# Kernel optimization log

Hardware: AMD Instinct MI355X
Metric: run time of the kernel (lower is better)

The kernel has to match this reference:

```python
import jax, jax.numpy as jnp
import numpy as np


def _hungarian(cost):
    """Jonker-Volgenant shortest-augmenting-path LAP solver (minimum cost).

    Returns col_ind such that rows arange(n) are matched to columns col_ind,
    identical (in objective) to scipy.optimize.linear_sum_assignment.
    Runs on host numpy, mirroring the original's detach().cpu() + scipy path.
    """
    cost = np.asarray(cost, dtype=np.float64)
    n = cost.shape[0]
    INF = np.inf
    u = np.zeros(n + 1)
    v = np.zeros(n + 1)
    p = np.zeros(n + 1, dtype=np.int64)   # p[j]: row (1-based) assigned to column j
    way = np.zeros(n + 1, dtype=np.int64)
    for i in range(1, n + 1):
        p[0] = i
        j0 = 0
        minv = np.full(n + 1, INF)
        used = np.zeros(n + 1, dtype=bool)
        while True:
            used[j0] = True
            i0 = p[j0]
            # vectorized relaxation of reduced costs for all unused columns
            cur = cost[i0 - 1] - u[i0] - v[1:]
            free = ~used[1:]
            upd = free & (cur < minv[1:])
            minv[1:] = np.where(upd, cur, minv[1:])
            way[1:] = np.where(upd, j0, way[1:])
            cand = np.where(free, minv[1:], INF)
            j1 = int(np.argmin(cand)) + 1
            delta = cand[j1 - 1]
            u[p[used]] += delta
            v[used] -= delta
            minv[1:] = np.where(free, minv[1:] - delta, minv[1:])
            j0 = j1
            if p[j0] == 0:
                break
        # augment along the alternating path
        while j0:
            j1 = way[j0]
            p[j0] = p[j1]
            j0 = j1
    col = np.empty(n, dtype=np.int64)
    col[p[1:] - 1] = np.arange(n)
    return col


def setup_inputs() -> dict:
    key = jax.random.key(0)
    B, N = 64, 256
    D = jax.random.normal(key, (B, N, N), dtype=jnp.float32)
    return {"D": D}


def reference(D):
    # Host round-trip for the assignment, exactly as the torch module does
    # (D.detach().cpu().numpy() -> scipy LAP per batch element).
    Dn = np.asarray(jax.device_get(D))
    cols = np.stack([_hungarian(Dn[b]) for b in range(Dn.shape[0])])  # [B, N]
    idx = jnp.asarray(cols)[:, :, None]                               # [B, N, 1]
    # gather matched costs D[b, i, col[b, i]] and reduce: mean per batch, then mean
    matched = jnp.take_along_axis(D, idx, axis=2)[..., 0]             # [B, N]
    return matched.mean(axis=1).mean()
```

## Files before the change

kernel.cpp:

```cpp
#include <hip/hip_runtime.h>

#define N_DIM 256
#define BATCH 64
#define BS 64
#define SCALE 4096.0f

#define DPP_MINU(x, ctrl) do {                                                 \
    unsigned _s = (unsigned)__builtin_amdgcn_update_dpp((int)(x), (int)(x),    \
                                                        (ctrl), 0xf, 0xf, false); \
    (x) = ((x) < _s) ? (x) : _s;                                               \
} while (0)

__device__ __forceinline__ unsigned wave_min_u32(unsigned x) {
    DPP_MINU(x, 0x111);
    DPP_MINU(x, 0x112);
    DPP_MINU(x, 0x114);
    DPP_MINU(x, 0x118);
    const unsigned a = (unsigned)__builtin_amdgcn_readlane((int)x, 15);
    const unsigned b = (unsigned)__builtin_amdgcn_readlane((int)x, 31);
    const unsigned c = (unsigned)__builtin_amdgcn_readlane((int)x, 47);
    const unsigned d = (unsigned)__builtin_amdgcn_readlane((int)x, 63);
    const unsigned ab = (a < b) ? a : b;
    const unsigned cd = (c < d) ? c : d;
    return (ab < cd) ? ab : cd;
}

__device__ __forceinline__ int rd4_i(int x0, int x1, int x2, int x3, int idx) {
    const int sel = idx & 3, src = idx >> 2;
    int ab = (sel & 1) ? x1 : x0;
    int cd = (sel & 1) ? x3 : x2;
    int vv = (sel & 2) ? cd : ab;
    return __builtin_amdgcn_readlane(vv, src);
}

#define SET4(x0, x1, x2, x3, idx, val) do {                                    \
    const int _sel = (idx) & 3;                                                \
    if (t == ((idx) >> 2)) {                                                   \
        if (_sel == 0) x0 = (val); else if (_sel == 1) x1 = (val);             \
        else if (_sel == 2) x2 = (val); else x3 = (val);                       \
    }                                                                          \
} while (0)

#define SET_GUARD(idx) do {                                                    \
    if (t == ((idx) >> 2)) {                                                   \
        const int _s = (idx) & 3;                                              \
        if (_s == 0) g0 = 0x7FFFFFFF; else if (_s == 1) g1 = 0x7FFFFFFF;       \
        else if (_s == 2) g2 = 0x7FFFFFFF; else g3 = 0x7FFFFFFF;               \
    }                                                                          \
} while (0)

#define RELAX(hh, addv, predrow) do {                                          \
    int r_, kn_;                                                               \
    r_  = (addv) + lo16((hh).x) + vn0;                                         \
    kn_ = (r_ << 8) | c0i; if (kn_ < k0) { p0 = (predrow); k0 = kn_; }         \
    r_  = (addv) + hi16((hh).x) + vn1;                                         \
    kn_ = (r_ << 8) | c1i; if (kn_ < k1) { p1 = (predrow); k1 = kn_; }         \
    r_  = (addv) + lo16((hh).y) + vn2;                                         \
    kn_ = (r_ << 8) | c2i; if (kn_ < k2) { p2 = (predrow); k2 = kn_; }         \
    r_  = (addv) + hi16((hh).y) + vn3;                                         \
    kn_ = (r_ << 8) | c3i; if (kn_ < k3) { p3 = (predrow); k3 = kn_; }         \
} while (0)

__device__ __forceinline__ int lo16(int p) { return (int)(short)(p & 0xFFFF); }
__device__ __forceinline__ int hi16(int p) { return p >> 16; }

__global__ __launch_bounds__(BS) void lap_kernel(const float* __restrict__ Dm,
                                                 double* __restrict__ batch_sums) {
    const int b = blockIdx.x;
    const int t = threadIdx.x;
    const float* __restrict__ cost = Dm + (size_t)b * N_DIM * N_DIM;
    const float4* __restrict__ cost4 = (const float4*)cost;

    __shared__ int2     chi[N_DIM * BS];
    __shared__ int      u_s[N_DIM];
    __shared__ int      v_s[N_DIM];
    __shared__ int      row4col_s[N_DIM];
    __shared__ int      col4row_s[N_DIM];
    __shared__ int      queue_s[N_DIM];
    __shared__ unsigned bid_s[N_DIM];
    __shared__ int      qcnt_s;

    const int c0i = 4 * t, c1i = 4 * t + 1, c2i = 4 * t + 2, c3i = 4 * t + 3;

    int cmn0 = INT_MAX, cmn1 = INT_MAX, cmn2 = INT_MAX, cmn3 = INT_MAX;
    int ca0 = 0, ca1 = 0, ca2 = 0, ca3 = 0;
    for (int r = 0; r < N_DIM; ++r) {
        const float4 c4 = cost4[r * BS + t];
        const int a0 = __float2int_rn(c4.x * SCALE);
        const int a1 = __float2int_rn(c4.y * SCALE);
        const int a2 = __float2int_rn(c4.z * SCALE);
        const int a3 = __float2int_rn(c4.w * SCALE);
        int2 p;
        p.x = (a0 & 0xFFFF) | (a1 << 16);
        p.y = (a2 & 0xFFFF) | (a3 << 16);
        chi[r * BS + t] = p;
        if (a0 < cmn0) { cmn0 = a0; ca0 = r; }
        if (a1 < cmn1) { cmn1 = a1; ca1 = r; }
        if (a2 < cmn2) { cmn2 = a2; ca2 = r; }
        if (a3 < cmn3) { cmn3 = a3; ca3 = r; }
    }
    {
        int4 vv; vv.x = cmn0; vv.y = cmn1; vv.z = cmn2; vv.w = cmn3;
        ((int4*)v_s)[t] = vv;
        int4 zz; zz.x = 0; zz.y = 0; zz.z = 0; zz.w = 0;
        ((int4*)u_s)[t] = zz;
        int4 mm; mm.x = -1; mm.y = -1; mm.z = -1; mm.w = -1;
        ((int4*)row4col_s)[t] = mm;
        ((int4*)col4row_s)[t] = mm;
        int4 rc; rc.x = 0x7fffffff; rc.y = 0x7fffffff; rc.z = 0x7fffffff; rc.w = 0x7fffffff;
        ((int4*)queue_s)[t] = rc;
        uint4 bb; bb.x = ~0u; bb.y = ~0u; bb.z = ~0u; bb.w = ~0u;
        ((uint4*)bid_s)[t] = bb;
    }
    __syncthreads();
    atomicMin(&queue_s[ca0], c0i);
    atomicMin(&queue_s[ca1], c1i);
    atomicMin(&queue_s[ca2], c2i);
    atomicMin(&queue_s[ca3], c3i);
    __syncthreads();
    if (queue_s[ca0] == c0i) { row4col_s[c0i] = ca0; col4row_s[ca0] = c0i; }
    if (queue_s[ca1] == c1i) { row4col_s[c1i] = ca1; col4row_s[ca1] = c1i; }
    if (queue_s[ca2] == c2i) { row4col_s[c2i] = ca2; col4row_s[ca2] = c2i; }
    if (queue_s[ca3] == c3i) { row4col_s[c3i] = ca3; col4row_s[ca3] = c3i; }
    __syncthreads();

    for (int pass = 0; pass < 12; ++pass) {
        if (t == 0) qcnt_s = 0;
        __syncthreads();
        {
            const int4 my = ((const int4*)col4row_s)[t];
            const int nf = (my.x < 0) + (my.y < 0) + (my.z < 0) + (my.w < 0);
            if (nf) {
                int pos = atomicAdd(&qcnt_s, nf);
                if (my.x < 0) queue_s[pos++] = c0i;
                if (my.y < 0) queue_s[pos++] = c1i;
                if (my.z < 0) queue_s[pos++] = c2i;
                if (my.w < 0) queue_s[pos++] = c3i;
            }
        }
        __syncthreads();
        const int n = qcnt_s;
        if (n == 0) break;
        for (int base = 0; base < n; base += BS) {
            const int my_row = (base + t < n) ? queue_s[base + t] : -1;
            int d1 = INT_MAX, d2 = INT_MAX;
            int j1 = 0;
            if (my_row >= 0) {
                const int rb = my_row * BS;
                for (int l = 0; l < BS; ++l) {
                    const int l2 = (l + t) & 63;
                    const int2 h = chi[rb + l2];
                    const int4 vv = ((const int4*)v_s)[l2];
                    int d;
                    d = lo16(h.x) - vv.x; if (d < d1) { d2 = d1; d1 = d; j1 = 4 * l2 + 0; } else if (d < d2) d2 = d;
                    d = hi16(h.x) - vv.y; if (d < d1) { d2 = d1; d1 = d; j1 = 4 * l2 + 1; } else if (d < d2) d2 = d;
                    d = lo16(h.y) - vv.z; if (d < d1) { d2 = d1; d1 = d; j1 = 4 * l2 + 2; } else if (d < d2) d2 = d;
                    d = hi16(h.y) - vv.w; if (d < d1) { d2 = d1; d1 = d; j1 = 4 * l2 + 3; } else if (d < d2) d2 = d;
                }
                atomicMin(&bid_s[j1], ((unsigned)d1 << 8) | (unsigned)t);
            }
            __syncthreads();
            if (my_row >= 0) {
                const unsigned mybid = ((unsigned)d1 << 8) | (unsigned)t;
                if (bid_s[j1] == mybid) {
                    const int i0 = row4col_s[j1];
                    row4col_s[j1] = my_row;
                    col4row_s[my_row] = j1;
                    if (i0 >= 0) col4row_s[i0] = -1;
                    u_s[my_row] = d2;
                    v_s[j1] += d1 - d2;
                    bid_s[j1] = ~0u;
                }
            }
            __syncthreads();
        }
    }

    const int4 vv4 = ((const int4*)v_s)[t];
    int vn0 = -vv4.x, vn1 = -vv4.y, vn2 = -vv4.z, vn3 = -vv4.w;
    const int4 m4 = ((const int4*)row4col_s)[t];
    int r4c0 = m4.x, r4c1 = m4.y, r4c2 = m4.z, r4c3 = m4.w;
    const int4 y4 = ((const int4*)col4row_s)[t];
    int c4r0 = y4.x, c4r1 = y4.y, c4r2 = y4.z, c4r3 = y4.w;
    int p0 = 0, p1 = 0, p2 = 0, p3 = 0;

    unsigned long long fm0 = __ballot(c4r0 < 0);
    unsigned long long fm1 = __ballot(c4r1 < 0);
    unsigned long long fm2 = __ballot(c4r2 < 0);
    unsigned long long fm3 = __ballot(c4r3 < 0);

    const int KINIT0 = (0x7FFFFF << 8) | c0i;
    const int KINIT1 = (0x7FFFFF << 8) | c1i;
    const int KINIT2 = (0x7FFFFF << 8) | c2i;
    const int KINIT3 = (0x7FFFFF << 8) | c3i;

    while (fm0 | fm1 | fm2 | fm3) {
        int i;
        if (fm0)      { const int tt = __builtin_ctzll(fm0); fm0 &= fm0 - 1; i = tt * 4 + 0; }
        else if (fm1) { const int tt = __builtin_ctzll(fm1); fm1 &= fm1 - 1; i = tt * 4 + 1; }
        else if (fm2) { const int tt = __builtin_ctzll(fm2); fm2 &= fm2 - 1; i = tt * 4 + 2; }
        else          { const int tt = __builtin_ctzll(fm3); fm3 &= fm3 - 1; i = tt * 4 + 3; }

        int k0 = KINIT0, k1 = KINIT1, k2 = KINIT2, k3 = KINIT3;
        int g0 = 0, g1 = 0, g2 = 0, g3 = 0;
        int minVal = 0;
        int sink = -1;

        {
            const int2 hS = chi[i * BS + t];
            const int  uS = u_s[i];
            RELAX(hS, -uS, i);
        }

        while (true) {
            int q0 = k0 | g0, q1 = k1 | g1, q2 = k2 | g2, q3 = k3 | g3;
            int q01 = (q0 < q1) ? q0 : q1;
            int q23 = (q2 < q3) ? q2 : q3;
            const int gk1 = (int)wave_min_u32((unsigned)((q01 < q23) ? q01 : q23));
            const int bi1 = gk1 & 0xFF;
            SET_GUARD(bi1);
            const int r41 = rd4_i(r4c0, r4c1, r4c2, r4c3, bi1);
            if (r41 < 0) { sink = bi1; minVal = gk1 >> 8; break; }

            const int2 h1 = chi[r41 * BS + t];
            const int  u1 = u_s[r41];

            q0 = k0 | g0; q1 = k1 | g1; q2 = k2 | g2; q3 = k3 | g3;
            q01 = (q0 < q1) ? q0 : q1;
            q23 = (q2 < q3) ? q2 : q3;
            const int gk2 = (int)wave_min_u32((unsigned)((q01 < q23) ? q01 : q23));
            const int bi2 = gk2 & 0xFF;
            const int r42 = rd4_i(r4c0, r4c1, r4c2, r4c3, bi2);
            const int rr2 = (r42 < 0) ? 0 : r42;
            const int2 h2 = chi[rr2 * BS + t];
            const int  u2 = u_s[rr2];

            RELAX(h1, (gk1 >> 8) - u1, r41);

            const int n0 = k0 | g0, n1 = k1 | g1, n2 = k2 | g2, n3 = k3 | g3;
            const int n01 = (n0 < n1) ? n0 : n1;
            const int n23 = (n2 < n3) ? n2 : n3;
            const int nl  = (n01 < n23) ? n01 : n23;
            if (__ballot((unsigned)nl < (unsigned)gk2) == 0ull) {
                SET_GUARD(bi2);
                if (r42 < 0) { sink = bi2; minVal = gk2 >> 8; break; }
                RELAX(h2, (gk2 >> 8) - u2, r42);
            }
        }

        if (g0) { const int dv = minVal - (k0 >> 8); vn0 += dv; if (r4c0 >= 0) u_s[r4c0] += dv; }
        if (g1) { const int dv = minVal - (k1 >> 8); vn1 += dv; if (r4c1 >= 0) u_s[r4c1] += dv; }
        if (g2) { const int dv = minVal - (k2 >> 8); vn2 += dv; if (r4c2 >= 0) u_s[r4c2] += dv; }
        if (g3) { const int dv = minVal - (k3 >> 8); vn3 += dv; if (r4c3 >= 0) u_s[r4c3] += dv; }
        if (t == 0) u_s[i] += minVal;

        if (sink >= 0) {
            int jj = sink;
            while (true) {
                const int ii = rd4_i(p0, p1, p2, p3, jj);
                SET4(r4c0, r4c1, r4c2, r4c3, jj, ii);
                const int tmp = rd4_i(c4r0, c4r1, c4r2, c4r3, ii);
                SET4(c4r0, c4r1, c4r2, c4r3, ii, jj);
                jj = tmp;
                if (ii == i) break;
            }
        }
    }

    double s = 0.0;
    s += (double)cost[(size_t)(t * 4 + 0) * N_DIM + c4r0];
    s += (double)cost[(size_t)(t * 4 + 1) * N_DIM + c4r1];
    s += (double)cost[(size_t)(t * 4 + 2) * N_DIM + c4r2];
    s += (double)cost[(size_t)(t * 4 + 3) * N_DIM + c4r3];
    #pragma unroll
    for (int off = 32; off > 0; off >>= 1) s += __shfl_down(s, off);
    if (t == 0) batch_sums[b] = s;
}

__global__ void finalize_kernel(const double* __restrict__ batch_sums,
                                float* __restrict__ out) {
    const int t = threadIdx.x;
    double s = batch_sums[t];
    #pragma unroll
    for (int off = 32; off > 0; off >>= 1) s += __shfl_down(s, off);
    if (t == 0) out[0] = (float)(s / (double)((long long)BATCH * N_DIM));
}

extern "C" void kernel_launch(void* const* d_in, const int* in_sizes, int n_in,
                              void* d_out, int out_size, void* d_ws, size_t ws_size,
                              hipStream_t stream) {
    const float* Dm = (const float*)d_in[0];
    float* out = (float*)d_out;
    double* sums = (double*)d_ws;

    lap_kernel<<<BATCH, BS, 0, stream>>>(Dm, sums);
    finalize_kernel<<<1, 64, 0, stream>>>(sums, out);
}
```

Baseline: 822.9 us.

## Run multi-source shortest augmenting path from all free rows at once

```diff
diff --git a/kernel.cpp b/kernel.cpp
--- a/kernel.cpp
+++ b/kernel.cpp
@@ -4,6 +4,7 @@
 #define BATCH 64
 #define BS 64
 #define SCALE 4096.0f
+#define KBIAS (1 << 20)
 
 #define DPP_MINU(x, ctrl) do {                                                 \
     unsigned _s = (unsigned)__builtin_amdgcn_update_dpp((int)(x), (int)(x),    \
@@ -177,7 +178,8 @@
     }
 
     const int4 vv4 = ((const int4*)v_s)[t];
-    int vn0 = -vv4.x, vn1 = -vv4.y, vn2 = -vv4.z, vn3 = -vv4.w;
+    int vn0 = KBIAS - vv4.x, vn1 = KBIAS - vv4.y;
+    int vn2 = KBIAS - vv4.z, vn3 = KBIAS - vv4.w;
     const int4 m4 = ((const int4*)row4col_s)[t];
     int r4c0 = m4.x, r4c1 = m4.y, r4c2 = m4.z, r4c3 = m4.w;
     const int4 y4 = ((const int4*)col4row_s)[t];
@@ -195,74 +197,70 @@
     const int KINIT3 = (0x7FFFFF << 8) | c3i;
 
     while (fm0 | fm1 | fm2 | fm3) {
-        int i;
-        if (fm0)      { const int tt = __builtin_ctzll(fm0); fm0 &= fm0 - 1; i = tt * 4 + 0; }
-        else if (fm1) { const int tt = __builtin_ctzll(fm1); fm1 &= fm1 - 1; i = tt * 4 + 1; }
-        else if (fm2) { const int tt = __builtin_ctzll(fm2); fm2 &= fm2 - 1; i = tt * 4 + 2; }
-        else          { const int tt = __builtin_ctzll(fm3); fm3 &= fm3 - 1; i = tt * 4 + 3; }
-
         int k0 = KINIT0, k1 = KINIT1, k2 = KINIT2, k3 = KINIT3;
         int g0 = 0, g1 = 0, g2 = 0, g3 = 0;
-        int minVal = 0;
+        int minValB = 0;
         int sink = -1;
 
         {
-            const int2 hS = chi[i * BS + t];
-            const int  uS = u_s[i];
-            RELAX(hS, -uS, i);
+            unsigned long long s0 = fm0, s1 = fm1, s2 = fm2, s3 = fm3;
+            while (s0 | s1 | s2 | s3) {
+                int i;
+                if (s0)      { const int tt = __builtin_ctzll(s0); s0 &= s0 - 1; i = tt * 4 + 0; }
+                else if (s1) { const int tt = __builtin_ctzll(s1); s1 &= s1 - 1; i = tt * 4 + 1; }
+                else if (s2) { const int tt = __builtin_ctzll(s2); s2 &= s2 - 1; i = tt * 4 + 2; }
+                else         { const int tt = __builtin_ctzll(s3); s3 &= s3 - 1; i = tt * 4 + 3; }
+                const int2 hS = chi[i * BS + t];
+                const int  uS = u_s[i];
+                RELAX(hS, -uS, i);
+            }
         }
 
         while (true) {
-            int q0 = k0 | g0, q1 = k1 | g1, q2 = k2 | g2, q3 = k3 | g3;
-            int q01 = (q0 < q1) ? q0 : q1;
-            int q23 = (q2 < q3) ? q2 : q3;
-            const int gk1 = (int)wave_min_u32((unsigned)((q01 < q23) ? q01 : q23));
-            const int bi1 = gk1 & 0xFF;
-            SET_GUARD(bi1);
-            const int r41 = rd4_i(r4c0, r4c1, r4c2, r4c3, bi1);
-            if (r41 < 0) { sink = bi1; minVal = gk1 >> 8; break; }
-
-            const int2 h1 = chi[r41 * BS + t];
-            const int  u1 = u_s[r41];
-
-            q0 = k0 | g0; q1 = k1 | g1; q2 = k2 | g2; q3 = k3 | g3;
-            q01 = (q0 < q1) ? q0 : q1;
-            q23 = (q2 < q3) ? q2 : q3;
-            const int gk2 = (int)wave_min_u32((unsigned)((q01 < q23) ? q01 : q23));
-            const int bi2 = gk2 & 0xFF;
-            const int r42 = rd4_i(r4c0, r4c1, r4c2, r4c3, bi2);
-            const int rr2 = (r42 < 0) ? 0 : r42;
-            const int2 h2 = chi[rr2 * BS + t];
-            const int  u2 = u_s[rr2];
-
-            RELAX(h1, (gk1 >> 8) - u1, r41);
-
-            const int n0 = k0 | g0, n1 = k1 | g1, n2 = k2 | g2, n3 = k3 | g3;
-            const int n01 = (n0 < n1) ? n0 : n1;
-            const int n23 = (n2 < n3) ? n2 : n3;
-            const int nl  = (n01 < n23) ? n01 : n23;
-            if (__ballot((unsigned)nl < (unsigned)gk2) == 0ull) {
-                SET_GUARD(bi2);
-                if (r42 < 0) { sink = bi2; minVal = gk2 >> 8; break; }
-                RELAX(h2, (gk2 >> 8) - u2, r42);
-            }
-        }
-
-        if (g0) { const int dv = minVal - (k0 >> 8); vn0 += dv; if (r4c0 >= 0) u_s[r4c0] += dv; }
-        if (g1) { const int dv = minVal - (k1 >> 8); vn1 += dv; if (r4c1 >= 0) u_s[r4c1] += dv; }
-        if (g2) { const int dv = minVal - (k2 >> 8); vn2 += dv; if (r4c2 >= 0) u_s[r4c2] += dv; }
-        if (g3) { const int dv = minVal - (k3 >> 8); vn3 += dv; if (r4c3 >= 0) u_s[r4c3] += dv; }
-        if (t == 0) u_s[i] += minVal;
-
-        if (sink >= 0) {
+            const int q0 = k0 | g0, q1 = k1 | g1, q2 = k2 | g2, q3 = k3 | g3;
+            const int q01 = (q0 < q1) ? q0 : q1;
+            const int q23 = (q2 < q3) ? q2 : q3;
+            const int gk = (int)wave_min_u32((unsigned)((q01 < q23) ? q01 : q23));
+
+            const int bi = gk & 0xFF;
+            minValB = gk >> 8;
+            const int r4 = rd4_i(r4c0, r4c1, r4c2, r4c3, bi);
+            SET_GUARD(bi);
+            if (r4 < 0) { sink = bi; break; }
+
+            const int2 h   = chi[r4 * BS + t];
+            const int ucur = u_s[r4];
+            RELAX(h, minValB - KBIAS - ucur, r4);
+        }
+
+        if (g0) { const int dv = minValB - (k0 >> 8); vn0 += dv; if (r4c0 >= 0) u_s[r4c0] += dv; }
+        if (g1) { const int dv = minValB - (k1 >> 8); vn1 += dv; if (r4c1 >= 0) u_s[r4c1] += dv; }
+        if (g2) { const int dv = minValB - (k2 >> 8); vn2 += dv; if (r4c2 >= 0) u_s[r4c2] += dv; }
+        if (g3) { const int dv = minValB - (k3 >> 8); vn3 += dv; if (r4c3 >= 0) u_s[r4c3] += dv; }
+        {
+            const int mvt = minValB - KBIAS;
+            if (c4r0 < 0) u_s[c0i] += mvt;
+            if (c4r1 < 0) u_s[c1i] += mvt;
+            if (c4r2 < 0) u_s[c2i] += mvt;
+            if (c4r3 < 0) u_s[c3i] += mvt;
+        }
+
+        {
             int jj = sink;
             while (true) {
                 const int ii = rd4_i(p0, p1, p2, p3, jj);
                 SET4(r4c0, r4c1, r4c2, r4c3, jj, ii);
                 const int tmp = rd4_i(c4r0, c4r1, c4r2, c4r3, ii);
                 SET4(c4r0, c4r1, c4r2, c4r3, ii, jj);
+                if (tmp < 0) {
+                    const int tt_ = ii >> 2, kk_ = ii & 3;
+                    if (kk_ == 0) fm0 &= ~(1ull << tt_);
+                    else if (kk_ == 1) fm1 &= ~(1ull << tt_);
+                    else if (kk_ == 2) fm2 &= ~(1ull << tt_);
+                    else fm3 &= ~(1ull << tt_);
+                    break;
+                }
                 jj = tmp;
-                if (ii == i) break;
             }
         }
     }
```

After: 914.1 us. +11.1%, slower.
